# Kernel tuning notes

Hardware: AMD Instinct MI355X
Metric: run time of the kernel (lower is better)

Reference implementation:

```python
import jax, jax.numpy as jnp
import numpy as np

D_MODEL = 512
HIDDEN = 2 * D_MODEL
B, L = 8, 2048
R_MIN, R_MAX = 0.8, 0.99
LN_EPS = 1e-5


def setup_inputs() -> dict:
    key = jax.random.key(0)
    ks = jax.random.split(key, 12)
    x = jax.random.normal(ks[0], (B, L, D_MODEL), jnp.float32)
    mask = jnp.ones((B, L), jnp.float32)
    # LRU eigenvalue init, exactly as the torch __init__
    u1 = jax.random.uniform(ks[1], (HIDDEN,), jnp.float32)
    u2 = jax.random.uniform(ks[2], (HIDDEN,), jnp.float32)
    nu_log = jnp.log(-0.5 * jnp.log(u1 * (R_MAX ** 2 - R_MIN ** 2) + R_MIN ** 2))
    theta_log = jnp.log(u2 * 2.0 * np.pi)
    diag_lambda = jnp.exp(jax.lax.complex(-jnp.exp(nu_log), jnp.exp(theta_log)))
    gamma_log = jnp.log(jnp.sqrt(1.0 - jnp.abs(diag_lambda) ** 2))
    params_log = jnp.stack([nu_log, theta_log, gamma_log])  # (3, HIDDEN)
    s_in = 1.0 / np.sqrt(D_MODEL)
    s_out = 1.0 / np.sqrt(HIDDEN)
    # complex Linear weights (real+imag parts; trained weights are fully complex)
    W_in_re = jax.random.uniform(ks[3], (HIDDEN, D_MODEL), jnp.float32, -s_in, s_in)
    W_in_im = jax.random.uniform(ks[4], (HIDDEN, D_MODEL), jnp.float32, -s_in, s_in)
    b_in_re = jax.random.uniform(ks[5], (HIDDEN,), jnp.float32, -s_in, s_in)
    b_in_im = jax.random.uniform(ks[6], (HIDDEN,), jnp.float32, -s_in, s_in)
    W_out_re = jax.random.uniform(ks[7], (D_MODEL, HIDDEN), jnp.float32, -s_out, s_out)
    W_out_im = jax.random.uniform(ks[8], (D_MODEL, HIDDEN), jnp.float32, -s_out, s_out)
    b_out_re = jax.random.uniform(ks[9], (D_MODEL,), jnp.float32, -s_out, s_out)
    b_out_im = jax.random.uniform(ks[10], (D_MODEL,), jnp.float32, -s_out, s_out)
    ln_w = jnp.ones((D_MODEL,), jnp.float32)
    ln_b = jnp.zeros((D_MODEL,), jnp.float32)
    return dict(x=x, mask=mask, params_log=params_log,
                W_in_re=W_in_re, W_in_im=W_in_im, b_in_re=b_in_re, b_in_im=b_in_im,
                W_out_re=W_out_re, W_out_im=W_out_im, b_out_re=b_out_re, b_out_im=b_out_im,
                ln_w=ln_w, ln_b=ln_b)


def _lru_parallel_scan(h, lamb, mask, Bn, Ln, Dn):
    # log-depth doubling trick over complex diagonal recurrence (faithful port)
    log2_L = int(np.ceil(np.log2(Ln)))
    for i in range(1, log2_L + 1):
        l = 2 ** i
        h = h.reshape(Bn * Ln // l, l, Dn)
        m = mask.reshape(Bn * Ln // l, l)
        h1, h2 = h[:, : l // 2], h[:, l // 2 :]
        if i > 1:
            lamb = jnp.concatenate([lamb, lamb * lamb[-1]], axis=0)  # powers lam^1..lam^(l/2)
        h2 = h2 + lamb * h1[:, -1:] * m[:, l // 2 - 1 : l // 2, None]
        h = jnp.concatenate([h1, h2], axis=1)
    return h.reshape(Bn, Ln, Dn)


def reference(x, mask, params_log, W_in_re, W_in_im, b_in_re, b_in_im,
              W_out_re, W_out_im, b_out_re, b_out_im, ln_w, ln_b):
    nu, theta, gamma = jnp.exp(params_log)  # each (HIDDEN,)
    lamb = jnp.exp(jax.lax.complex(-nu, theta))[None, :]  # (1, HIDDEN)
    W_in = jax.lax.complex(W_in_re, W_in_im)
    b_in = jax.lax.complex(b_in_re, b_in_im)
    W_out = jax.lax.complex(W_out_re, W_out_im)
    b_out = jax.lax.complex(b_out_re, b_out_im)
    xc = x.astype(jnp.complex64)
    h = (jnp.einsum('bld,hd->blh', xc, W_in) + b_in) * gamma  # (B, L, HIDDEN) complex64
    Bn, Ln, Dn = h.shape
    h = _lru_parallel_scan(h, lamb, mask, Bn, Ln, Dn)
    y = (jnp.einsum('blh,dh->bld', h, W_out) + b_out).real + x  # dropout = identity (eval)
    mean = jnp.mean(y, axis=-1, keepdims=True)
    var = jnp.var(y, axis=-1, keepdims=True)
    return (y - mean) / jnp.sqrt(var + LN_EPS) * ln_w + ln_b
```

## Files before the change

kernel.cpp:

```cpp
#include <hip/hip_runtime.h>
#include <hip/hip_bf16.h>
#include <cstdint>
#include <cstddef>


typedef unsigned short u16;
typedef __attribute__((ext_vector_type(8))) short bf16x8;
typedef __attribute__((ext_vector_type(4))) float f32x4;

#define B_    8
#define L_    2048
#define D_    512
#define H_    1024
#define M_    (B_ * L_)
#define SEG_  64
#define T_    (L_ / SEG_)

__device__ __forceinline__ float b2f(u16 u) {
  union { unsigned int i; float f; } v; v.i = ((unsigned int)u) << 16; return v.f;
}
__device__ __forceinline__ u16 f2b(float f) {
  union { float f; unsigned int i; } v; v.f = f;
  unsigned int x = v.i;
  return (u16)((x + 0x7fffu + ((x >> 16) & 1u)) >> 16);
}

__device__ __forceinline__ void gl2lds16(const void* g, void* l) {
  __builtin_amdgcn_global_load_lds(
      (const __attribute__((address_space(1))) void*)g,
      (__attribute__((address_space(3))) void*)l, 16, 0, 0);
}

__device__ __forceinline__ int ksw8(int row, int c) {
  return (c ^ (row & 7)) & 7;
}

__global__ __launch_bounds__(256) void prep_all(
    const float* __restrict__ x, u16* __restrict__ xb,
    const float* __restrict__ wire, const float* __restrict__ wiim,
    const float* __restrict__ wore, const float* __restrict__ woim,
    const float* __restrict__ bire, const float* __restrict__ biim,
    const float* __restrict__ params,
    u16* __restrict__ winb, u16* __restrict__ wcat, float* __restrict__ bb)
{
  int i = blockIdx.x * 256 + threadIdx.x;
#pragma unroll
  for (int j = 0; j < 4; ++j) {
    int gi = i + j * 524288;
    float4 v = ((const float4*)x)[gi];
    ushort4 o;
    o.x = f2b(v.x); o.y = f2b(v.y); o.z = f2b(v.z); o.w = f2b(v.w);
    ((ushort4*)xb)[gi] = o;
  }
  {
    int cp = i >> 9, k = i & 511;
    float g = expf(params[2 * H_ + cp]);
    winb[(size_t)(2 * cp) * 512 + k]     = f2b(wire[i] * g);
    winb[(size_t)(2 * cp + 1) * 512 + k] = f2b(wiim[i] * g);
  }
  {
    int d = i >> 10, c = i & 1023;
    wcat[(size_t)d * 2048 + 2 * c]     = f2b(wore[i]);
    wcat[(size_t)d * 2048 + 2 * c + 1] = f2b(-woim[i]);
  }
  if (i < 1024) {
    float gb = expf(params[2 * H_ + i]);
    bb[2 * i]     = bire[i] * gb;
    bb[2 * i + 1] = biim[i] * gb;
  }
}

__global__ __launch_bounds__(256, 4) void gemm_scan(
    const u16* __restrict__ A, const u16* __restrict__ Bp,
    const float* __restrict__ mask, const float* __restrict__ params,
    u16* __restrict__ h, const float* __restrict__ bb,
    float2* __restrict__ segfin, float* __restrict__ prodm)
{
  __shared__ __align__(16) u16 sAB[16384];
  __shared__ float mf[128];
  const int K = 512;

  const int tid  = threadIdx.x;
  const int lane = tid & 63;
  const int wave = tid >> 6;
  const int wm = wave >> 1, wn = wave & 1;
  const int m0 = blockIdx.x * 128;
  const int n0 = blockIdx.y * 128;
  const int b  = m0 >> 11;
  const int local0 = m0 & (L_ - 1);

  f32x4 acc[4][4];
#pragma unroll
  for (int i = 0; i < 4; ++i)
#pragma unroll
    for (int j = 0; j < 4; ++j) { f32x4 z = {0.f, 0.f, 0.f, 0.f}; acc[i][j] = z; }

  const int q = lane >> 4;
  const int r = lane & 15;

  for (int k0 = 0; k0 < K; k0 += 64) {
#pragma unroll
    for (int it = 0; it < 4; ++it) {
      int ci  = it * 256 + tid;
      int row = ci >> 3;
      int kc  = ksw8(row, ci & 7);
      gl2lds16(A  + (size_t)(m0 + row) * K + k0 + kc * 8, &sAB[ci * 8]);
      gl2lds16(Bp + (size_t)(n0 + row) * K + k0 + kc * 8, &sAB[8192 + ci * 8]);
    }
    __syncthreads();
#pragma unroll
    for (int kk = 0; kk < 2; ++kk) {
      const int cs = kk * 4 + q;
      bf16x8 af[4], bfv[4];
#pragma unroll
      for (int mt = 0; mt < 4; ++mt) {
        int arow = wm * 64 + mt * 16 + r;
        af[mt] = *(const bf16x8*)&sAB[(arow * 8 + ksw8(arow, cs)) * 8];
      }
#pragma unroll
      for (int nt = 0; nt < 4; ++nt) {
        int brow = wn * 64 + nt * 16 + r;
        bfv[nt] = *(const bf16x8*)&sAB[8192 + (brow * 8 + ksw8(brow, cs)) * 8];
      }
#pragma unroll
      for (int mt = 0; mt < 4; ++mt)
#pragma unroll
        for (int nt = 0; nt < 4; ++nt)
          acc[mt][nt] = __builtin_amdgcn_mfma_f32_16x16x32_bf16(
              bfv[nt], af[mt], acc[mt][nt], 0, 0, 0);
    }
    __syncthreads();
  }

  u16* sH = sAB;
  if (tid < 128)
    mf[tid] = (local0 + tid == 0) ? 0.f
                                  : mask[b * L_ + local0 + tid - 1];
#pragma unroll
  for (int mt = 0; mt < 4; ++mt) {
    const int trow = wm * 64 + mt * 16 + r;
    const int sw = (trow & 7) << 4;
#pragma unroll
    for (int nt = 0; nt < 4; ++nt) {
      const int nc = wn * 64 + nt * 16 + q * 4;
      const float4 b4 = *(const float4*)&bb[n0 + nc];
      ushort4 o;
      o.x = f2b(acc[mt][nt][0] + b4.x);
      o.y = f2b(acc[mt][nt][1] + b4.y);
      o.z = f2b(acc[mt][nt][2] + b4.z);
      o.w = f2b(acc[mt][nt][3] + b4.w);
      *(ushort4*)&sH[trow * 128 + (nc ^ sw)] = o;
    }
  }
  __syncthreads();

#pragma unroll
  for (int it = 0; it < 8; ++it) {
    int flat = it * 256 + tid;
    int row  = flat >> 4;
    int c16  = (flat & 15) * 8;
    bf16x8 v = *(const bf16x8*)&sH[row * 128 + (c16 ^ ((row & 7) << 4))];
    *(bf16x8*)&h[(size_t)(m0 + row) * 2048 + n0 + c16] = v;
  }

  {
    const int sIdx = wave;
    const int cpG  = (n0 >> 1) + lane;
    float nu = expf(params[cpG]);
    float th = expf(params[H_ + cpG]);
    float mg = expf(-nu);
    float lr = mg * cosf(th), li = mg * sinf(th);
    float sr = 0.f, si = 0.f, pm = 1.f;
    const int rbase = sIdx * 32;
#pragma unroll
    for (int t = 0; t < 32; ++t) {
      int row = rbase + t;
      int pos = row * 128 + ((lane * 2) ^ ((row & 7) << 4));
      ushort2 v = *(const ushort2*)&sH[pos];
      float fac = mf[row];
      pm *= fac;
      float nr = b2f(v.x) + fac * (lr * sr - li * si);
      float ni = b2f(v.y) + fac * (lr * si + li * sr);
      sr = nr; si = ni;
    }
    const int sG = (local0 >> 5) + sIdx;
    segfin[(size_t)(b * SEG_ + sG) * H_ + cpG] = make_float2(sr, si);
    if (lane == 0 && n0 == 0) prodm[b * SEG_ + sG] = pm;
  }
}

__global__ __launch_bounds__(256) void scan_carry(
    const float2* __restrict__ segfin, const float* __restrict__ prodm,
    const float* __restrict__ params, float2* __restrict__ carries)
{
  int idx = blockIdx.x * 256 + threadIdx.x;
  int b = idx >> 10, cp = idx & 1023;
  float nu = expf(params[cp]);
  float th = expf(params[H_ + cp]);
  float mg = expf(-nu);
  float ltr = mg * cosf(th), lti = mg * sinf(th);
#pragma unroll
  for (int sq = 0; sq < 5; ++sq) {
    float nr = ltr * ltr - lti * lti;
    float ni = 2.f * ltr * lti;
    ltr = nr; lti = ni;
  }
  float cr = 0.f, ci = 0.f;
  float2 fin = segfin[(size_t)(b * SEG_) * H_ + cp];
  float pmv = prodm[b * SEG_];
  for (int s = 0; s < SEG_; ++s) {
    size_t o = (size_t)(b * SEG_ + s) * H_ + cp;
    carries[o] = make_float2(cr, ci);
    float2 finn; float pmn;
    if (s + 1 < SEG_) { finn = segfin[o + H_]; pmn = prodm[b * SEG_ + s + 1]; }
    float nr = fin.x + pmv * (ltr * cr - lti * ci);
    float ni = fin.y + pmv * (ltr * ci + lti * cr);
    cr = nr; ci = ni;
    fin = finn; pmv = pmn;
  }
}

__global__ __launch_bounds__(256) void scan_full(
    u16* __restrict__ h, const float* __restrict__ mask,
    const float* __restrict__ params, const float2* __restrict__ carries)
{
  const int s = blockIdx.x, b = blockIdx.y;
  const int pa = threadIdx.x * 4;
  float lr[4], li[4], sr[4], si[4];
#pragma unroll
  for (int j = 0; j < 4; ++j) {
    int cp = pa + j;
    float nu = expf(params[cp]);
    float th = expf(params[H_ + cp]);
    float mg = expf(-nu);
    lr[j] = mg * cosf(th);
    li[j] = mg * sinf(th);
    float2 cv = carries[(size_t)(b * SEG_ + s) * H_ + cp];
    sr[j] = cv.x; si[j] = cv.y;
  }
  const int t0 = s * T_;
  u16* p = h + (size_t)(b * L_ + t0) * 2048 + pa * 2;
  const float* mp = mask + b * L_ + t0;
  float fac0;
  if (t0 == 0) fac0 = 0.f; else fac0 = mask[b * L_ + t0 - 1];

  bf16x8 buf[2][8];
#pragma unroll
  for (int j = 0; j < 8; ++j)
    buf[0][j] = *(const bf16x8*)(p + (size_t)j * 2048);
#pragma unroll
  for (int ch = 0; ch < T_ / 8; ++ch) {
    const int cur = ch & 1, nxt = cur ^ 1;
    if (ch < T_ / 8 - 1) {
      u16* pn = p + (size_t)(ch + 1) * 8 * 2048;
#pragma unroll
      for (int j = 0; j < 8; ++j)
        buf[nxt][j] = *(const bf16x8*)(pn + (size_t)j * 2048);
    }
#pragma unroll
    for (int j = 0; j < 8; ++j) {
      int i = ch * 8 + j;
      float fac = (i == 0) ? fac0 : mp[i - 1];
      u16 vv[8], ov[8];
      *(bf16x8*)vv = buf[cur][j];
#pragma unroll
      for (int k = 0; k < 4; ++k) {
        float ar = fac * sr[k], ai = fac * si[k];
        float nr = b2f(vv[2 * k])     + lr[k] * ar - li[k] * ai;
        float ni = b2f(vv[2 * k + 1]) + lr[k] * ai + li[k] * ar;
        sr[k] = nr; si[k] = ni;
        ov[2 * k]     = f2b(nr);
        ov[2 * k + 1] = f2b(ni);
      }
      *(bf16x8*)(p + (size_t)i * 2048) = *(bf16x8*)ov;
    }
  }
}

__global__ __launch_bounds__(512, 2) void gemm2_ln(
    const u16* __restrict__ A, const u16* __restrict__ Bp,
    const float* __restrict__ xg, const float* __restrict__ p0,
    const float* __restrict__ lnw, const float* __restrict__ lnb,
    float* __restrict__ out)
{
  __shared__ __align__(16) u16 sA[2][64 * 64];
  __shared__ __align__(16) u16 sB[2][512 * 64];
  __shared__ float red_s[4][64], red_ss[4][64];

  const int K = 2048;
  const int tid  = threadIdx.x;
  const int lane = tid & 63;
  const int wave = tid >> 6;
  const int wm = wave >> 2;
  const int wn = wave & 3;
  const int m0 = blockIdx.x * 64;
  const int q = lane >> 4;
  const int r = lane & 15;

  f32x4 acc[2][8];
#pragma unroll
  for (int i = 0; i < 2; ++i)
#pragma unroll
    for (int j = 0; j < 8; ++j) { f32x4 z = {0.f, 0.f, 0.f, 0.f}; acc[i][j] = z; }

  auto stage = [&](int bsel, int k0) {
    {
      int ci  = tid;
      int row = ci >> 3;
      int kc  = ksw8(row, ci & 7);
      gl2lds16(A + (size_t)(m0 + row) * K + k0 + kc * 8, &sA[bsel][ci * 8]);
    }
#pragma unroll
    for (int it = 0; it < 8; ++it) {
      int ci  = it * 512 + tid;
      int row = ci >> 3;
      int kc  = ksw8(row, ci & 7);
      gl2lds16(Bp + (size_t)row * K + k0 + kc * 8, &sB[bsel][ci * 8]);
    }
  };

  stage(0, 0);
  __syncthreads();

  for (int t = 0; t < 32; ++t) {
    const int cur = t & 1;
    if (t < 31) stage(cur ^ 1, (t + 1) * 64);
#pragma unroll
    for (int kk = 0; kk < 2; ++kk) {
      const int cs = kk * 4 + q;
      bf16x8 af[2], bfv[8];
#pragma unroll
      for (int mt = 0; mt < 2; ++mt) {
        int arow = wm * 32 + mt * 16 + r;
        af[mt] = *(const bf16x8*)&sA[cur][(arow * 8 + ksw8(arow, cs)) * 8];
      }
#pragma unroll
      for (int nt = 0; nt < 8; ++nt) {
        int brow = wn * 128 + nt * 16 + r;
        bfv[nt] = *(const bf16x8*)&sB[cur][(brow * 8 + ksw8(brow, cs)) * 8];
      }
#pragma unroll
      for (int mt = 0; mt < 2; ++mt)
#pragma unroll
        for (int nt = 0; nt < 8; ++nt)
          acc[mt][nt] = __builtin_amdgcn_mfma_f32_16x16x32_bf16(
              bfv[nt], af[mt], acc[mt][nt], 0, 0, 0);
    }
    __syncthreads();
  }

  float s[2] = {0.f, 0.f}, ss[2] = {0.f, 0.f};
#pragma unroll
  for (int mt = 0; mt < 2; ++mt) {
    const size_t grow = (size_t)(m0 + wm * 32 + mt * 16 + r);
#pragma unroll
    for (int nt = 0; nt < 8; ++nt) {
      const int c4 = wn * 128 + nt * 16 + q * 4;
      const float4 b4 = *(const float4*)&p0[c4];
      const float4 x4 = *(const float4*)&xg[grow * 512 + c4];
      acc[mt][nt][0] += b4.x + x4.x;
      acc[mt][nt][1] += b4.y + x4.y;
      acc[mt][nt][2] += b4.z + x4.z;
      acc[mt][nt][3] += b4.w + x4.w;
#pragma unroll
      for (int j = 0; j < 4; ++j) {
        float z = acc[mt][nt][j];
        s[mt] += z; ss[mt] += z * z;
      }
    }
  }
#pragma unroll
  for (int mt = 0; mt < 2; ++mt) {
    s[mt]  += __shfl_xor(s[mt], 16);  s[mt]  += __shfl_xor(s[mt], 32);
    ss[mt] += __shfl_xor(ss[mt], 16); ss[mt] += __shfl_xor(ss[mt], 32);
  }
  if (q == 0) {
#pragma unroll
    for (int mt = 0; mt < 2; ++mt) {
      const int lr_ = wm * 32 + mt * 16 + r;
      red_s[wn][lr_]  = s[mt];
      red_ss[wn][lr_] = ss[mt];
    }
  }
  __syncthreads();
#pragma unroll
  for (int mt = 0; mt < 2; ++mt) {
    const int lr_ = wm * 32 + mt * 16 + r;
    const float S  = red_s[0][lr_] + red_s[1][lr_] + red_s[2][lr_] + red_s[3][lr_];
    const float SS = red_ss[0][lr_] + red_ss[1][lr_] + red_ss[2][lr_] + red_ss[3][lr_];
    const float mean = S * (1.f / 512.f);
    const float var  = SS * (1.f / 512.f) - mean * mean;
    const float inv  = rsqrtf(var + 1e-5f);
    const size_t grow = (size_t)(m0 + lr_);
#pragma unroll
    for (int nt = 0; nt < 8; ++nt) {
      const int c4 = wn * 128 + nt * 16 + q * 4;
      const float4 w4 = *(const float4*)&lnw[c4];
      const float4 g4 = *(const float4*)&lnb[c4];
      float4 o;
      o.x = (acc[mt][nt][0] - mean) * inv * w4.x + g4.x;
      o.y = (acc[mt][nt][1] - mean) * inv * w4.y + g4.y;
      o.z = (acc[mt][nt][2] - mean) * inv * w4.z + g4.z;
      o.w = (acc[mt][nt][3] - mean) * inv * w4.w + g4.w;
      *(float4*)&out[grow * 512 + c4] = o;
    }
  }
}

extern "C" void kernel_launch(void* const* d_in, const int* in_sizes, int n_in,
                              void* d_out, int out_size, void* d_ws, size_t ws_size,
                              hipStream_t stream) {
  (void)in_sizes; (void)n_in; (void)out_size; (void)ws_size;
  const float* x      = (const float*)d_in[0];
  const float* mask   = (const float*)d_in[1];
  const float* params = (const float*)d_in[2];
  const float* Wire   = (const float*)d_in[3];
  const float* Wiim   = (const float*)d_in[4];
  const float* bire   = (const float*)d_in[5];
  const float* biim   = (const float*)d_in[6];
  const float* Wore   = (const float*)d_in[7];
  const float* Woim   = (const float*)d_in[8];
  const float* bore   = (const float*)d_in[9];
  const float* lnw    = (const float*)d_in[11];
  const float* lnb    = (const float*)d_in[12];

  char* ws = (char*)d_ws;
  u16*    xb      = (u16*)   (ws);
  float2* segfin  = (float2*)(ws + (size_t)16777216);
  float2* carries = (float2*)(ws + (size_t)20971520);
  float*  prodm   = (float*) (ws + (size_t)25165824);
  u16*    h       = (u16*)   (ws + (size_t)33554432);
  u16*    winb    = (u16*)   (ws + (size_t)100663296);
  u16*    wcat    = (u16*)   (ws + (size_t)102760448);
  float*  bb      = (float*) (ws + (size_t)104857600);

  prep_all<<<2048, 256, 0, stream>>>(x, xb, Wire, Wiim, Wore, Woim,
                                     bire, biim, params, winb, wcat, bb);

  gemm_scan<<<dim3(128, 16), 256, 0, stream>>>(
      xb, winb, mask, params, h, bb, segfin, prodm);

  scan_carry<<<32, 256, 0, stream>>>(segfin, prodm, params, carries);
  scan_full<<<dim3(SEG_, B_), 256, 0, stream>>>(h, mask, params, carries);

  gemm2_ln<<<256, 512, 0, stream>>>(h, wcat, x, bore, lnw, lnb, (float*)d_out);
}
```

Baseline: 241.8 us.

## Restructure output GEMM into per-wave private B pipelines with register-held A

The gemm2_ln kernel is reorganised so each of the 8 waves owns a 64-column slice of the output and double-buffers its own B tiles in a private LDS region. A fragments are loaded straight from global memory into registers. The block-wide __syncthreads in the K loop is replaced by per-wave vmcnt/lgkmcnt waits and sched barriers, which removes cross-wave synchronisation stalls. The cost is more register pressure from the 4x4 accumulators plus two sets of A fragments, uncoalesced global A loads repeated by every wave, and a larger 128KB LDS footprint that may limit occupancy.

```diff
diff --git a/kernel.cpp b/kernel.cpp
--- a/kernel.cpp
+++ b/kernel.cpp
@@ -283,79 +283,113 @@
     const float* __restrict__ lnw, const float* __restrict__ lnb,
     float* __restrict__ out)
 {
-  __shared__ __align__(16) u16 sA[2][64 * 64];
-  __shared__ __align__(16) u16 sB[2][512 * 64];
-  __shared__ float red_s[4][64], red_ss[4][64];
+  __shared__ __align__(16) u16 smem[65536];
 
   const int K = 2048;
   const int tid  = threadIdx.x;
   const int lane = tid & 63;
   const int wave = tid >> 6;
-  const int wm = wave >> 2;
-  const int wn = wave & 3;
   const int m0 = blockIdx.x * 64;
   const int q = lane >> 4;
   const int r = lane & 15;
 
-  f32x4 acc[2][8];
-#pragma unroll
-  for (int i = 0; i < 2; ++i)
-#pragma unroll
-    for (int j = 0; j < 8; ++j) { f32x4 z = {0.f, 0.f, 0.f, 0.f}; acc[i][j] = z; }
-
-  auto stage = [&](int bsel, int k0) {
-    {
-      int ci  = tid;
-      int row = ci >> 3;
-      int kc  = ksw8(row, ci & 7);
-      gl2lds16(A + (size_t)(m0 + row) * K + k0 + kc * 8, &sA[bsel][ci * 8]);
-    }
-#pragma unroll
-    for (int it = 0; it < 8; ++it) {
-      int ci  = it * 512 + tid;
-      int row = ci >> 3;
-      int kc  = ksw8(row, ci & 7);
-      gl2lds16(Bp + (size_t)row * K + k0 + kc * 8, &sB[bsel][ci * 8]);
+  u16* myB0 = smem + wave * 8192;
+  u16* myB1 = myB0 + 4096;
+  const u16* Aw = A + (size_t)m0 * K;
+  const u16* Bw = Bp + (size_t)(wave * 64) * K;
+
+  f32x4 acc[4][4];
+#pragma unroll
+  for (int i = 0; i < 4; ++i)
+#pragma unroll
+    for (int j = 0; j < 4; ++j) { f32x4 z = {0.f, 0.f, 0.f, 0.f}; acc[i][j] = z; }
+
+  auto stage_b = [&](u16* dst, int k0) {
+#pragma unroll
+    for (int j = 0; j < 8; ++j) {
+      int cj  = j * 64 + lane;
+      int row = cj >> 3;
+      int c   = (cj ^ row) & 7;
+      gl2lds16(Bw + (size_t)row * K + k0 + c * 8, dst + cj * 8);
     }
   };
-
-  stage(0, 0);
-  __syncthreads();
-
-  for (int t = 0; t < 32; ++t) {
-    const int cur = t & 1;
-    if (t < 31) stage(cur ^ 1, (t + 1) * 64);
+  auto load_a = [&](bf16x8 (&dst)[2][4], int k0) {
+#pragma unroll
+    for (int kk = 0; kk < 2; ++kk)
+#pragma unroll
+      for (int mt = 0; mt < 4; ++mt)
+        dst[kk][mt] = *(const bf16x8*)&Aw[(size_t)(mt * 16 + r) * K + k0
+                                          + (kk * 4 + q) * 8];
+  };
+  auto compute_tile = [&](const u16* buf, bf16x8 (&afc)[2][4]) {
 #pragma unroll
     for (int kk = 0; kk < 2; ++kk) {
       const int cs = kk * 4 + q;
-      bf16x8 af[2], bfv[8];
-#pragma unroll
-      for (int mt = 0; mt < 2; ++mt) {
-        int arow = wm * 32 + mt * 16 + r;
-        af[mt] = *(const bf16x8*)&sA[cur][(arow * 8 + ksw8(arow, cs)) * 8];
+      bf16x8 bfv[4];
+#pragma unroll
+      for (int nt = 0; nt < 4; ++nt) {
+        int brow = nt * 16 + r;
+        bfv[nt] = *(const bf16x8*)&buf[(brow * 8 + ksw8(brow, cs)) * 8];
       }
 #pragma unroll
-      for (int nt = 0; nt < 8; ++nt) {
-        int brow = wn * 128 + nt * 16 + r;
-        bfv[nt] = *(const bf16x8*)&sB[cur][(brow * 8 + ksw8(brow, cs)) * 8];
-      }
-#pragma unroll
-      for (int mt = 0; mt < 2; ++mt)
-#pragma unroll
-        for (int nt = 0; nt < 8; ++nt)
+      for (int mt = 0; mt < 4; ++mt)
+#pragma unroll
+        for (int nt = 0; nt < 4; ++nt)
           acc[mt][nt] = __builtin_amdgcn_mfma_f32_16x16x32_bf16(
-              bfv[nt], af[mt], acc[mt][nt], 0, 0, 0);
-    }
-    __syncthreads();
-  }
-
-  float s[2] = {0.f, 0.f}, ss[2] = {0.f, 0.f};
-#pragma unroll
-  for (int mt = 0; mt < 2; ++mt) {
-    const size_t grow = (size_t)(m0 + wm * 32 + mt * 16 + r);
-#pragma unroll
-    for (int nt = 0; nt < 8; ++nt) {
-      const int c4 = wn * 128 + nt * 16 + q * 4;
+              bfv[nt], afc[kk][mt], acc[mt][nt], 0, 0, 0);
+    }
+  };
+
+#define VM16  asm volatile("s_waitcnt vmcnt(16)" ::: "memory"); \
+              __builtin_amdgcn_sched_barrier(0)
+#define VM8   asm volatile("s_waitcnt vmcnt(8)"  ::: "memory"); \
+              __builtin_amdgcn_sched_barrier(0)
+#define LGKM0 asm volatile("s_waitcnt lgkmcnt(0)" ::: "memory"); \
+              __builtin_amdgcn_sched_barrier(0)
+
+  bf16x8 af_a[2][4], af_b[2][4];
+
+  stage_b(myB0, 0);
+  __builtin_amdgcn_sched_barrier(0);
+  load_a(af_a, 0);
+  __builtin_amdgcn_sched_barrier(0);
+  stage_b(myB1, 64);
+  __builtin_amdgcn_sched_barrier(0);
+
+  for (int tt = 0; tt < 15; ++tt) {
+    const int t = tt * 2;
+    VM16; compute_tile(myB0, af_a); LGKM0;
+    load_a(af_b, (t + 1) * 64);
+    __builtin_amdgcn_sched_barrier(0);
+    stage_b(myB0, (t + 2) * 64);
+    __builtin_amdgcn_sched_barrier(0);
+
+    VM16; compute_tile(myB1, af_b); LGKM0;
+    load_a(af_a, (t + 2) * 64);
+    __builtin_amdgcn_sched_barrier(0);
+    stage_b(myB1, (t + 3) * 64);
+    __builtin_amdgcn_sched_barrier(0);
+  }
+  VM16; compute_tile(myB0, af_a); LGKM0;
+  load_a(af_b, 31 * 64);
+  __builtin_amdgcn_sched_barrier(0);
+  VM8;  compute_tile(myB1, af_b);
+
+#undef VM16
+#undef VM8
+#undef LGKM0
+
+  __syncthreads();
+  float* red_s  = (float*)smem;
+  float* red_ss = red_s + 512;
+
+  float s[4] = {0.f, 0.f, 0.f, 0.f}, ss[4] = {0.f, 0.f, 0.f, 0.f};
+#pragma unroll
+  for (int mt = 0; mt < 4; ++mt) {
+    const size_t grow = (size_t)(m0 + mt * 16 + r);
+#pragma unroll
+    for (int nt = 0; nt < 4; ++nt) {
+      const int c4 = wave * 64 + nt * 16 + q * 4;
       const float4 b4 = *(const float4*)&p0[c4];
       const float4 x4 = *(const float4*)&xg[grow * 512 + c4];
       acc[mt][nt][0] += b4.x + x4.x;
@@ -370,31 +404,35 @@
     }
   }
 #pragma unroll
-  for (int mt = 0; mt < 2; ++mt) {
+  for (int mt = 0; mt < 4; ++mt) {
     s[mt]  += __shfl_xor(s[mt], 16);  s[mt]  += __shfl_xor(s[mt], 32);
     ss[mt] += __shfl_xor(ss[mt], 16); ss[mt] += __shfl_xor(ss[mt], 32);
   }
   if (q == 0) {
 #pragma unroll
-    for (int mt = 0; mt < 2; ++mt) {
-      const int lr_ = wm * 32 + mt * 16 + r;
-      red_s[wn][lr_]  = s[mt];
-      red_ss[wn][lr_] = ss[mt];
+    for (int mt = 0; mt < 4; ++mt) {
+      const int lr_ = mt * 16 + r;
+      red_s[wave * 64 + lr_]  = s[mt];
+      red_ss[wave * 64 + lr_] = ss[mt];
     }
   }
   __syncthreads();
 #pragma unroll
-  for (int mt = 0; mt < 2; ++mt) {
-    const int lr_ = wm * 32 + mt * 16 + r;
-    const float S  = red_s[0][lr_] + red_s[1][lr_] + red_s[2][lr_] + red_s[3][lr_];
-    const float SS = red_ss[0][lr_] + red_ss[1][lr_] + red_ss[2][lr_] + red_ss[3][lr_];
+  for (int mt = 0; mt < 4; ++mt) {
+    const int lr_ = mt * 16 + r;
+    float S = 0.f, SS = 0.f;
+#pragma unroll
+    for (int w = 0; w < 8; ++w) {
+      S  += red_s[w * 64 + lr_];
+      SS += red_ss[w * 64 + lr_];
+    }
     const float mean = S * (1.f / 512.f);
     const float var  = SS * (1.f / 512.f) - mean * mean;
     const float inv  = rsqrtf(var + 1e-5f);
     const size_t grow = (size_t)(m0 + lr_);
 #pragma unroll
-    for (int nt = 0; nt < 8; ++nt) {
-      const int c4 = wn * 128 + nt * 16 + q * 4;
+    for (int nt = 0; nt < 4; ++nt) {
+      const int c4 = wave * 64 + nt * 16 + q * 4;
       const float4 w4 = *(const float4*)&lnw[c4];
       const float4 g4 = *(const float4*)&lnb[c4];
       float4 o;
```

After: 279.8 us. 15.7% more time.
